# Performance work log

Measured on AMD Instinct MI355X. Metric: run time of the kernel, lower is better.

## Reference

```python
import jax, jax.numpy as jnp
import numpy as np

GAMMA = 0.002  # init kwarg
N, M, D = 8192, 8192, 512


def setup_inputs() -> dict:
    key = jax.random.key(0)
    kx, ky = jax.random.split(key)
    x = jax.random.normal(kx, (N, D), dtype=jnp.float32)
    y = jax.random.normal(ky, (M, D), dtype=jnp.float32)
    return {"x": x, "y": y}


def reference(x, y):
    # k(x, y) = exp(-gamma * ||x - y||^2), using the GEMM identity
    x = x.reshape(-1, x.shape[-1])
    y = y.reshape(-1, y.shape[-1])
    x_sq = jnp.sum(x * x, axis=-1)          # [N]
    y_sq = jnp.sum(y * y, axis=-1)          # [M]
    xy = jnp.einsum('nd,md->nm', x, y)      # [N, M] GEMM
    sq_dist = x_sq[:, None] + y_sq[None, :] - 2.0 * xy
    sq_dist = jnp.maximum(sq_dist, 0.0)     # clamp fp cancellation
    return jnp.exp(-jnp.float32(GAMMA) * sq_dist)
```

## Files before the change

kernel.cpp:

```cpp
#include <hip/hip_runtime.h>
#include <hip/hip_bf16.h>

#define GAMMA 0.002f
#define NROWS 8192
#define MROWS 8192
#define DDIM  512

typedef __attribute__((ext_vector_type(8))) short bf16x8;
typedef __attribute__((ext_vector_type(4))) float f32x4;
typedef __attribute__((ext_vector_type(8))) unsigned short ushort8;

static __device__ __forceinline__ unsigned short f32_to_bf16_rne(float f) {
    unsigned int u = __float_as_uint(f);
    unsigned int lsb = (u >> 16) & 1u;
    u += 0x7fffu + lsb;
    return (unsigned short)(u >> 16);
}

__global__ __launch_bounds__(64) void prep_kernel(const float* __restrict__ src,
                                                  unsigned short* __restrict__ dstb,
                                                  float* __restrict__ sq) {
    const int row  = blockIdx.x;
    const int lane = threadIdx.x;

    const float4* p = (const float4*)(src + (size_t)row * DDIM) + lane * 2;
    float4 f0 = p[0];
    float4 f1 = p[1];

    float s = f0.x*f0.x + f0.y*f0.y + f0.z*f0.z + f0.w*f0.w
            + f1.x*f1.x + f1.y*f1.y + f1.z*f1.z + f1.w*f1.w;

    float t[8] = {f0.x, f0.y, f0.z, f0.w, f1.x, f1.y, f1.z, f1.w};
    ushort8 hv;
#pragma unroll
    for (int i = 0; i < 8; ++i) hv[i] = f32_to_bf16_rne(t[i]);
    *(ushort8*)(dstb + (size_t)row * DDIM + lane * 8) = hv;

#pragma unroll
    for (int off = 32; off > 0; off >>= 1) s += __shfl_down(s, off);
    if (lane == 0) sq[row] = s;
}

__global__ __launch_bounds__(256) void rbf_gemm_kernel(
        const unsigned short* __restrict__ xb,
        const unsigned short* __restrict__ yb,
        const float* __restrict__ xsq,
        const float* __restrict__ ysq,
        float* __restrict__ out) {
    __shared__ __align__(16) unsigned short smem[2 * 128 * 32];
    unsigned short* smemA = smem;
    unsigned short* smemB = smem + 128 * 32;

    const int tid  = threadIdx.x;
    const int wave = tid >> 6;
    const int lane = tid & 63;

    const int rowBase = blockIdx.x * 128;
    const int colBase = blockIdx.y * 128;

    const int wm = wave >> 1;
    const int wn = wave & 1;

    f32x4 acc[4][4];
#pragma unroll
    for (int i = 0; i < 4; ++i)
#pragma unroll
        for (int j = 0; j < 4; ++j) acc[i][j] = (f32x4){0.f, 0.f, 0.f, 0.f};

    const int srow = lane >> 2;
    const int skb  = (lane & 3) * 16;

    const int fr  = lane & 15;
    const int fkb = (lane >> 4) * 16;

    for (int kt = 0; kt < DDIM / 32; ++kt) {
        const int k0b = kt * 64;
#pragma unroll
        for (int r = 0; r < 2; ++r) {
            const int seg = r * 4 + wave;
            {
                const char* g = (const char*)xb
                    + ((size_t)(rowBase + seg * 16 + srow) * DDIM) * 2 + k0b + skb;
                __builtin_amdgcn_global_load_lds(
                    (__attribute__((address_space(1))) void*)g,
                    (__attribute__((address_space(3))) void*)((char*)smemA + seg * 1024),
                    16, 0, 0);
            }
            {
                const char* g = (const char*)yb
                    + ((size_t)(colBase + seg * 16 + srow) * DDIM) * 2 + k0b + skb;
                __builtin_amdgcn_global_load_lds(
                    (__attribute__((address_space(1))) void*)g,
                    (__attribute__((address_space(3))) void*)((char*)smemB + seg * 1024),
                    16, 0, 0);
            }
        }
        __syncthreads();

        bf16x8 a[4], b[4];
#pragma unroll
        for (int i = 0; i < 4; ++i)
            a[i] = *(const bf16x8*)((const char*)smemA + (wm * 64 + i * 16 + fr) * 64 + fkb);
#pragma unroll
        for (int j = 0; j < 4; ++j)
            b[j] = *(const bf16x8*)((const char*)smemB + (wn * 64 + j * 16 + fr) * 64 + fkb);

#pragma unroll
        for (int i = 0; i < 4; ++i)
#pragma unroll
            for (int j = 0; j < 4; ++j)
                acc[i][j] = __builtin_amdgcn_mfma_f32_16x16x32_bf16(a[i], b[j], acc[i][j], 0, 0, 0);

        __syncthreads();
    }

    const int q4 = (lane >> 4) * 4;
#pragma unroll
    for (int i = 0; i < 4; ++i) {
        float xr[4];
#pragma unroll
        for (int r2 = 0; r2 < 4; ++r2)
            xr[r2] = xsq[rowBase + wm * 64 + i * 16 + q4 + r2];
#pragma unroll
        for (int j = 0; j < 4; ++j) {
            const int gcol = colBase + wn * 64 + j * 16 + fr;
            const float yc = ysq[gcol];
#pragma unroll
            for (int r2 = 0; r2 < 4; ++r2) {
                const int grow = rowBase + wm * 64 + i * 16 + q4 + r2;
                float d = xr[r2] + yc - 2.0f * acc[i][j][r2];
                d = fmaxf(d, 0.0f);
                out[(size_t)grow * MROWS + gcol] = __expf(-GAMMA * d);
            }
        }
    }
}

extern "C" void kernel_launch(void* const* d_in, const int* in_sizes, int n_in,
                              void* d_out, int out_size, void* d_ws, size_t ws_size,
                              hipStream_t stream) {
    const float* x = (const float*)d_in[0];
    const float* y = (const float*)d_in[1];
    float* out = (float*)d_out;

    unsigned short* xb = (unsigned short*)d_ws;
    unsigned short* yb = xb + (size_t)NROWS * DDIM;
    float* xsq = (float*)(yb + (size_t)MROWS * DDIM);
    float* ysq = xsq + NROWS;

    prep_kernel<<<NROWS, 64, 0, stream>>>(x, xb, xsq);
    prep_kernel<<<MROWS, 64, 0, stream>>>(y, yb, ysq);

    dim3 grid(NROWS / 128, MROWS / 128);
    rbf_gemm_kernel<<<grid, 256, 0, stream>>>(xb, yb, xsq, ysq, out);
}
```

Before: 349.5 us.

## Rework GEMM into 256x256 double-buffered pipeline with swizzled LDS and block remap

Replaces the 128x128 single-buffered GEMM tile with a 256x256 tile over 512 threads and BK=64. Global-to-LDS loads are double-buffered and issued two stages ahead, synchronised with explicit vmcnt/lgkmcnt waits and barriers. LDS rows are XOR-swizzled to avoid bank conflicts, blocks are remapped for L2 locality, and MFMA sections run at raised wave priority. The aim is to hide load latency and raise arithmetic intensity, at the cost of 128KB of LDS per block and many more accumulator registers, which limits occupancy.

Measured after the change: 389.9 us. +11.6%, slower.

```diff
diff --git a/kernel.cpp b/kernel.cpp
--- a/kernel.cpp
+++ b/kernel.cpp
@@ -5,6 +5,11 @@
 #define NROWS 8192
 #define MROWS 8192
 #define DDIM  512
+
+#define BM 256
+#define BN 256
+#define BK 64
+#define KT (DDIM / BK)
 
 typedef __attribute__((ext_vector_type(8))) short bf16x8;
 typedef __attribute__((ext_vector_type(4))) float f32x4;
@@ -41,94 +46,127 @@
     if (lane == 0) sq[row] = s;
 }
 
-__global__ __launch_bounds__(256) void rbf_gemm_kernel(
+__global__ __launch_bounds__(512, 2) void rbf_gemm_kernel(
         const unsigned short* __restrict__ xb,
         const unsigned short* __restrict__ yb,
         const float* __restrict__ xsq,
         const float* __restrict__ ysq,
         float* __restrict__ out) {
-    __shared__ __align__(16) unsigned short smem[2 * 128 * 32];
-    unsigned short* smemA = smem;
-    unsigned short* smemB = smem + 128 * 32;
+    __shared__ __align__(16) char smem[2 * 65536];
 
     const int tid  = threadIdx.x;
     const int wave = tid >> 6;
     const int lane = tid & 63;
 
-    const int rowBase = blockIdx.x * 128;
-    const int colBase = blockIdx.y * 128;
+    const int bid = (int)(blockIdx.y * gridDim.x + blockIdx.x);
+    const int swz = (bid & 7) * 128 + (bid >> 3);
+    const int rowBase = (swz & 31) * BM;
+    const int colBase = (swz >> 5) * BN;
 
-    const int wm = wave >> 1;
-    const int wn = wave & 1;
-
-    f32x4 acc[4][4];
-#pragma unroll
-    for (int i = 0; i < 4; ++i)
-#pragma unroll
-        for (int j = 0; j < 4; ++j) acc[i][j] = (f32x4){0.f, 0.f, 0.f, 0.f};
-
-    const int srow = lane >> 2;
-    const int skb  = (lane & 3) * 16;
+    const int wm = wave >> 2;
+    const int wn = wave & 3;
 
     const int fr  = lane & 15;
-    const int fkb = (lane >> 4) * 16;
+    const int kb0 = ((lane >> 4) << 4) ^ ((lane & 7) << 4);
+    const int kb1 = kb0 ^ 64;
 
-    for (int kt = 0; kt < DDIM / 32; ++kt) {
-        const int k0b = kt * 64;
+    const int aoff = (wm * 128 + fr) * 128;
+    const int boff = (wn * 64  + fr) * 128;
+
+    const int srow8 = lane >> 3;
+    const int sgsrc = ((lane & 7) ^ (lane >> 3)) << 4;
+    const size_t arowg = (size_t)(rowBase + wave * 32 + srow8) * (DDIM * 2);
+    const size_t browg = (size_t)(colBase + wave * 32 + srow8) * (DDIM * 2);
+    const char* xg = (const char*)xb;
+    const char* yg = (const char*)yb;
+    char* sm = (char*)smem;
+
+    f32x4 acc[8][4];
 #pragma unroll
-        for (int r = 0; r < 2; ++r) {
-            const int seg = r * 4 + wave;
-            {
-                const char* g = (const char*)xb
-                    + ((size_t)(rowBase + seg * 16 + srow) * DDIM) * 2 + k0b + skb;
-                __builtin_amdgcn_global_load_lds(
-                    (__attribute__((address_space(1))) void*)g,
-                    (__attribute__((address_space(3))) void*)((char*)smemA + seg * 1024),
-                    16, 0, 0);
-            }
-            {
-                const char* g = (const char*)yb
-                    + ((size_t)(colBase + seg * 16 + srow) * DDIM) * 2 + k0b + skb;
-                __builtin_amdgcn_global_load_lds(
-                    (__attribute__((address_space(1))) void*)g,
-                    (__attribute__((address_space(3))) void*)((char*)smemB + seg * 1024),
-                    16, 0, 0);
-            }
+    for (int m = 0; m < 8; ++m)
+#pragma unroll
+        for (int n = 0; n < 4; ++n) acc[m][n] = (f32x4){0.f, 0.f, 0.f, 0.f};
+
+    auto STAGE = [&](int kt, int c) {
+        const int kb = kt * 128 + sgsrc;
+#pragma unroll
+        for (int s = 0; s < 4; ++s) {
+            __builtin_amdgcn_global_load_lds(
+                (__attribute__((address_space(1))) void*)(xg + arowg + (size_t)s * 8192 + kb),
+                (__attribute__((address_space(3))) void*)(sm + c * 65536 + wave * 4096 + s * 1024),
+                16, 0, 0);
+            __builtin_amdgcn_global_load_lds(
+                (__attribute__((address_space(1))) void*)(yg + browg + (size_t)s * 8192 + kb),
+                (__attribute__((address_space(3))) void*)(sm + c * 65536 + 32768 + wave * 4096 + s * 1024),
+                16, 0, 0);
         }
-        __syncthreads();
+    };
 
-        bf16x8 a[4], b[4];
-#pragma unroll
-        for (int i = 0; i < 4; ++i)
-            a[i] = *(const bf16x8*)((const char*)smemA + (wm * 64 + i * 16 + fr) * 64 + fkb);
-#pragma unroll
-        for (int j = 0; j < 4; ++j)
-            b[j] = *(const bf16x8*)((const char*)smemB + (wn * 64 + j * 16 + fr) * 64 + fkb);
+    STAGE(0, 0);
+    asm volatile("" ::: "memory");
+    STAGE(1, 1);
+    asm volatile("s_waitcnt vmcnt(8)" ::: "memory");
+    __builtin_amdgcn_s_barrier();
+    asm volatile("" ::: "memory");
 
 #pragma unroll
-        for (int i = 0; i < 4; ++i)
+    for (int t = 0; t < KT; ++t) {
+        const int c = t & 1;
+        const char* smc = sm + c * 65536;
+        bf16x8 A0[8], B0[4], A1[8], B1[4];
+
 #pragma unroll
-            for (int j = 0; j < 4; ++j)
-                acc[i][j] = __builtin_amdgcn_mfma_f32_16x16x32_bf16(a[i], b[j], acc[i][j], 0, 0, 0);
+        for (int m = 0; m < 8; ++m) A0[m] = *(const bf16x8*)(smc + aoff + m * 2048 + kb0);
+#pragma unroll
+        for (int n = 0; n < 4; ++n) B0[n] = *(const bf16x8*)(smc + 32768 + boff + n * 2048 + kb0);
+        __builtin_amdgcn_s_setprio(1);
+#pragma unroll
+        for (int m = 0; m < 8; ++m)
+#pragma unroll
+            for (int n = 0; n < 4; ++n)
+                acc[m][n] = __builtin_amdgcn_mfma_f32_16x16x32_bf16(A0[m], B0[n], acc[m][n], 0, 0, 0);
+        __builtin_amdgcn_s_setprio(0);
 
-        __syncthreads();
+#pragma unroll
+        for (int m = 0; m < 8; ++m) A1[m] = *(const bf16x8*)(smc + aoff + m * 2048 + kb1);
+#pragma unroll
+        for (int n = 0; n < 4; ++n) B1[n] = *(const bf16x8*)(smc + 32768 + boff + n * 2048 + kb1);
+        asm volatile("s_waitcnt lgkmcnt(0)" ::: "memory");
+        __builtin_amdgcn_s_barrier();
+        asm volatile("" ::: "memory");
+
+        if (t + 2 < KT) STAGE(t + 2, c);
+
+        __builtin_amdgcn_s_setprio(1);
+#pragma unroll
+        for (int m = 0; m < 8; ++m)
+#pragma unroll
+            for (int n = 0; n < 4; ++n)
+                acc[m][n] = __builtin_amdgcn_mfma_f32_16x16x32_bf16(A1[m], B1[n], acc[m][n], 0, 0, 0);
+        __builtin_amdgcn_s_setprio(0);
+
+        if (t + 2 < KT)      { asm volatile("s_waitcnt vmcnt(8)" ::: "memory"); }
+        else if (t + 1 < KT) { asm volatile("s_waitcnt vmcnt(0)" ::: "memory"); }
+        __builtin_amdgcn_s_barrier();
+        asm volatile("" ::: "memory");
     }
 
     const int q4 = (lane >> 4) * 4;
+    const int rb = rowBase + wm * 128;
+    const int cb = colBase + wn * 64;
 #pragma unroll
-    for (int i = 0; i < 4; ++i) {
+    for (int m = 0; m < 8; ++m) {
         float xr[4];
 #pragma unroll
-        for (int r2 = 0; r2 < 4; ++r2)
-            xr[r2] = xsq[rowBase + wm * 64 + i * 16 + q4 + r2];
+        for (int r2 = 0; r2 < 4; ++r2) xr[r2] = xsq[rb + m * 16 + q4 + r2];
 #pragma unroll
-        for (int j = 0; j < 4; ++j) {
-            const int gcol = colBase + wn * 64 + j * 16 + fr;
-            const float yc = ysq[gcol];
+        for (int n = 0; n < 4; ++n) {
+            const int gcol = cb + n * 16 + fr;
+            const float ysq_c = ysq[gcol];
 #pragma unroll
             for (int r2 = 0; r2 < 4; ++r2) {
-                const int grow = rowBase + wm * 64 + i * 16 + q4 + r2;
-                float d = xr[r2] + yc - 2.0f * acc[i][j][r2];
+                const int grow = rb + m * 16 + q4 + r2;
+                float d = xr[r2] + ysq_c - 2.0f * acc[m][n][r2];
                 d = fmaxf(d, 0.0f);
                 out[(size_t)grow * MROWS + gcol] = __expf(-GAMMA * d);
             }
@@ -151,6 +189,6 @@
     prep_kernel<<<NROWS, 64, 0, stream>>>(x, xb, xsq);
     prep_kernel<<<MROWS, 64, 0, stream>>>(y, yb, ysq);
 
-    dim3 grid(NROWS / 128, MROWS / 128);
-    rbf_gemm_kernel<<<grid, 256, 0, stream>>>(xb, yb, xsq, ysq, out);
+    dim3 grid(NROWS / BM, MROWS / BN);
+    rbf_gemm_kernel<<<grid, 512, 0, stream>>>(xb, yb, xsq, ysq, out);
 }
```
